# Kernel optimization log

Hardware: AMD Instinct MI355X
Metric: run time of the kernel (lower is better)

## Reference

```python
import jax, jax.numpy as jnp
import numpy as np
from jax import lax


def _quadrature_weights(bw):
    # s2cnn-style Driscoll-Healy quadrature weights over beta, length 2*bw
    j = np.arange(2 * bw)
    k = np.arange(bw)
    theta = np.pi * (2 * j + 1) / (4 * bw)
    s = (np.sin(np.outer(2 * j + 1, 2 * k + 1) * np.pi / (4 * bw)) / (2 * k + 1)).sum(-1)
    return jnp.asarray((2.0 / bw) * np.sin(theta) * s, jnp.float32)


def _conv2d(x, W, b):
    y = lax.conv_general_dilated(x, W, (1, 1), 'SAME',
                                 dimension_numbers=('NCHW', 'OIHW', 'NCHW'))
    return y + b[None, :, None, None]


def setup_inputs() -> dict:
    key = jax.random.key(0)
    ks = jax.random.split(key, 8)
    b, n = 8, 32768
    res_pt, res_r = 32, 8
    inputs = jax.random.normal(ks[0], (b, n, 3), jnp.float32)
    return {
        'inputs': inputs,
        'scale': jnp.float32(3.0),      # max radius covered by radial bins
        'sigma': jnp.float32(0.5),      # gaussian width in grid units
        'A': jnp.float32(1.0),          # splat amplitude
        'inteval_comp': jnp.float32(0.5),
        'res_pt': res_pt,
        'res_r': res_r,
        'W_s2_1': 0.08 * jax.random.normal(ks[1], (32, 8, 3, 3), jnp.float32),
        'b_s2_1': jnp.zeros((32,), jnp.float32),
        'W_s2_2': 0.05 * jax.random.normal(ks[2], (64, 32, 3, 3), jnp.float32),
        'b_s2_2': jnp.zeros((64,), jnp.float32),
        'W_gamma': 0.1 * jax.random.normal(ks[3], (64, 32), jnp.float32),
        'W_c3_1': 0.05 * jax.random.normal(ks[4], (64, 128), jnp.float32),
        'b_c3_1': jnp.zeros((64,), jnp.float32),
        'W_c3_2': 0.05 * jax.random.normal(ks[5], (32, 64), jnp.float32),
        'b_c3_2': jnp.zeros((32,), jnp.float32),
    }


def reference(inputs, scale, sigma, A, inteval_comp, res_pt, res_r,
              W_s2_1, b_s2_1, W_s2_2, b_s2_2, W_gamma,
              W_c3_1, b_c3_1, W_c3_2, b_c3_2):
    b, n, _ = inputs.shape
    # ---- remap: cartesian -> spherical with min-radius clamp (utils.remap) ----
    x, y, z = inputs[..., 0], inputs[..., 1], inputs[..., 2]
    r = jnp.maximum(jnp.sqrt(x * x + y * y + z * z), 0.1)
    theta = jnp.arccos(jnp.clip(z / r, -1.0, 1.0))            # [0, pi]
    phi = jnp.arctan2(y, x) + np.pi                            # [0, 2pi)
    # ---- s2_gridding: gaussian-weighted point -> (theta,phi,r) grid scatter ----
    ct = theta / np.pi * res_pt                                # continuous bin coords
    cp = phi / (2 * np.pi) * res_pt
    cr = r / scale * res_r
    it = jnp.clip(jnp.floor(ct).astype(jnp.int32), 0, res_pt - 1)
    ip = jnp.clip(jnp.floor(cp).astype(jnp.int32), 0, res_pt - 1)
    ir = jnp.clip(jnp.floor(cr).astype(jnp.int32), 0, res_r - 1)
    d2 = ((ct - (it + inteval_comp)) ** 2
          + (cp - (ip + inteval_comp)) ** 2
          + (cr - (ir + inteval_comp)) ** 2)
    w = A * jnp.exp(-d2 / (2.0 * sigma * sigma))               # (b, n)
    vals = jnp.stack([w, w * x, w * y, w * z], axis=-1)        # (b, n, 4)
    bidx = jnp.arange(b, dtype=jnp.int32)[:, None] * jnp.ones((1, n), jnp.int32)
    flat = ((bidx * res_pt + it) * res_pt + ip) * res_r + ir   # (b, n)
    grid = jnp.zeros((b * res_pt * res_pt * res_r, 4), jnp.float32)
    grid = grid.at[flat.reshape(-1)].add(vals.reshape(-1, 4))
    grid = grid.reshape(b, res_pt, res_pt, res_r, 4)
    ft = jnp.transpose(grid[..., 0], (0, 3, 1, 2))             # (b, res_r, res_pt, res_pt)
    # ---- encoder_l1 (s2cnn_equators): S2 convs + gamma lift to SO3 grid ----
    h = jax.nn.relu(_conv2d(ft, W_s2_1, b_s2_1))
    h = jax.nn.relu(_conv2d(h, W_s2_2, b_s2_2))                # (b, 64, res_pt, res_pt)
    ft_grid = jnp.einsum('bcxy,cg->bcxyg', h, W_gamma)         # (b, 64, rp, rp, rp)
    # ---- so3_integrate: quadrature weight over beta, sum alpha/gamma ----
    wq = _quadrature_weights(res_pt // 2)                      # (res_pt,)
    ft_max = jnp.einsum('bcxyg,y->bc', ft_grid, wq)            # (b, 64)
    # ---- broadcast global feature, concat, pointwise conv3d head ----
    ft_max_ = jnp.broadcast_to(ft_max[:, :, None, None, None],
                               (b, ft_grid.shape[1], res_pt, res_pt, res_pt))
    cat = jnp.concatenate([ft_grid, ft_max_], axis=1)          # (b, 128, rp, rp, rp)
    h3 = jax.nn.relu(jnp.einsum('bcxyg,dc->bdxyg', cat, W_c3_1)
                     + b_c3_1[None, :, None, None, None])
    out = (jnp.einsum('bdxyg,ed->bexyg', h3, W_c3_2)
           + b_c3_2[None, :, None, None, None])                # (b, 32, rp, rp, rp)
    ft_g = out.reshape(b, out.shape[1], -1).max(-1)            # (b, 32)
    return (out, ft_g)
```

## Files before the change

kernel.cpp:

```cpp
#include <hip/hip_runtime.h>
#include <math.h>

#define PI_D 3.14159265358979323846
#define PI_F 3.14159265358979323846f

typedef _Float16 half8 __attribute__((ext_vector_type(8)));
typedef _Float16 half4v __attribute__((ext_vector_type(4)));
typedef float floatx4 __attribute__((ext_vector_type(4)));
#define MFMA16(a,b,c) __builtin_amdgcn_mfma_f32_16x16x32_f16(a,b,c,0,0,0)

__global__ void k_scatter(const float* __restrict__ inp,
                          const float* __restrict__ p_scale,
                          const float* __restrict__ p_sigma,
                          const float* __restrict__ p_A,
                          const float* __restrict__ p_ic,
                          const float* __restrict__ Wg,
                          float* __restrict__ ft, float* __restrict__ wq,
                          float* __restrict__ sgs, float* __restrict__ WS) {
  int blk = blockIdx.x, t = threadIdx.x;
  if (blk == 0) {
    if (t < 32) {
      double jj = 2.0*(double)t + 1.0;
      double theta = PI_D * jj / 64.0;
      double s = 0.0;
      for (int k = 0; k < 16; ++k)
        s += sin(jj * (double)(2*k+1) * PI_D / 64.0) / (double)(2*k+1);
      wq[t] = (float)((2.0/16.0) * sin(theta) * s);
    } else if (t < 96) {
      int c = t - 32;
      float s = 0.f;
      for (int g = 0; g < 32; ++g) s += Wg[c*32 + g];
      sgs[c] = s;
    } else if (t < 224) {
      ((float4*)WS)[t - 96] = make_float4(0.f, 0.f, 0.f, 0.f);
    }
  }
  int i = blk * 256 + t;
  float scale = p_scale[0];
  float sigma = p_sigma[0];
  float A     = p_A[0];
  float icomp = p_ic[0];
  int b = i >> 15;
  float x = inp[i*3+0];
  float y = inp[i*3+1];
  float z = inp[i*3+2];
  float r = sqrtf(x*x + y*y + z*z);
  r = fmaxf(r, 0.1f);
  float ctv = fminf(fmaxf(z / r, -1.0f), 1.0f);
  float theta = acosf(ctv);
  float phi = atan2f(y, x) + PI_F;
  float ct = theta * (32.0f / PI_F);
  float cp = phi * (32.0f / (2.0f * PI_F));
  float cr = r / scale * 8.0f;
  int it = (int)floorf(ct); it = min(max(it, 0), 31);
  int ip = (int)floorf(cp); ip = min(max(ip, 0), 31);
  int ir = (int)floorf(cr); ir = min(max(ir, 0), 7);
  float dt = ct - ((float)it + icomp);
  float dp = cp - ((float)ip + icomp);
  float dr = cr - ((float)ir + icomp);
  float d2 = dt*dt + dp*dp + dr*dr;
  float w = A * expf(-d2 / (2.0f * sigma * sigma));
  atomicAdd(&ft[((b*8 + ir)*32 + it)*32 + ip], w);
}

__global__ __launch_bounds__(512) void k_conv12(
    const float* __restrict__ ft, const float* __restrict__ W1,
    const float* __restrict__ b1, const float* __restrict__ W2,
    const float* __restrict__ b2, const float* __restrict__ wq,
    const float* __restrict__ Wg, const float* __restrict__ Wc31,
    const float* __restrict__ Wc32,
    _Float16* __restrict__ VswH, _Float16* __restrict__ VswL,
    _Float16* __restrict__ W2swH, _Float16* __restrict__ W2swL,
    float* __restrict__ h2, float* __restrict__ WS) {
  __shared__ __align__(16) float ftt[8][5][32];
  __shared__ __align__(16) float h1t[32][3][32];
  __shared__ __align__(16) float W1s[72*33];
  __shared__ __align__(16) float W2s[288*65];
  int blk = blockIdx.x;
  int b = blk >> 5, xt = blk & 31;
  int t = threadIdx.x;

  {
    int flat = blk * 512 + t;
    int jj = flat & 7;
    int l  = (flat >> 3) & 63;
    int rest = flat >> 9;
    int ks = rest & 1, mt = rest >> 1;
    int c = ks*32 + (l >> 4)*8 + jj;
    int m = mt*16 + (l & 15);
    int g = m >> 6, d = m & 63;
    float val = Wg[c*32 + g] * Wc31[d*128 + c];
    _Float16 hi = (_Float16)val;
    VswH[flat] = hi;
    VswL[flat] = (_Float16)(val - (float)hi);
    if (flat < 2048) {
      int ks2 = rest & 1, mt2 = rest >> 1;
      int e = mt2*16 + (l & 15);
      int dd = ks2*32 + (l >> 4)*8 + jj;
      float v2 = Wc32[e*64 + dd];
      _Float16 h2i = (_Float16)v2;
      W2swH[flat] = h2i;
      W2swL[flat] = (_Float16)(v2 - (float)h2i);
    }
  }

  for (int idx = t; idx < 2304; idx += 512) {
    int oc2 = idx / 72, rest = idx % 72;
    W1s[rest*33 + oc2] = W1[idx];
  }
  for (int idx = t; idx < 4608; idx += 512) {
    float4 v4 = ((const float4*)W2)[idx];
    int base = idx * 4;
    int oc = base / 288, r0 = base % 288;
    W2s[(r0+0)*65 + oc] = v4.x;
    W2s[(r0+1)*65 + oc] = v4.y;
    W2s[(r0+2)*65 + oc] = v4.z;
    W2s[(r0+3)*65 + oc] = v4.w;
  }
  for (int idx = t; idx < 1280; idx += 512) {
    int y = idx & 31, xx = (idx >> 5) % 5, ic = idx / 160;
    int xg = xt + xx - 2;
    ftt[ic][xx][y] = ((unsigned)xg < 32u) ? ft[b*8192 + ic*1024 + xg*32 + y] : 0.f;
  }
  __syncthreads();

  {
    int y = t & 31, grp = t >> 5;
    float acc[2][3];
    float bb0 = b1[grp*2+0], bb1 = b1[grp*2+1];
#pragma unroll
    for (int xr = 0; xr < 3; ++xr) { acc[0][xr] = bb0; acc[1][xr] = bb1; }
    for (int ic = 0; ic < 8; ++ic) {
      float v[5][3];
#pragma unroll
      for (int dyi = 0; dyi < 3; ++dyi) {
        int yy = y + dyi - 1;
        bool ok = ((unsigned)yy < 32u);
        int yc = min(max(yy, 0), 31);
#pragma unroll
        for (int xx = 0; xx < 5; ++xx) {
          float tv = ftt[ic][xx][yc];
          v[xx][dyi] = ok ? tv : 0.f;
        }
      }
#pragma unroll
      for (int k = 0; k < 9; ++k) {
        float w0 = W1s[(ic*9 + k)*33 + grp*2];
        float w1 = W1s[(ic*9 + k)*33 + grp*2 + 1];
        int dx = k / 3, dy = k % 3;
#pragma unroll
        for (int xr = 0; xr < 3; ++xr) {
          float vv = v[xr + dx][dy];
          acc[0][xr] = fmaf(vv, w0, acc[0][xr]);
          acc[1][xr] = fmaf(vv, w1, acc[1][xr]);
        }
      }
    }
#pragma unroll
    for (int xr = 0; xr < 3; ++xr) {
      int xg = xt + xr - 1;
      bool ok = ((unsigned)xg < 32u);
      h1t[grp*2+0][xr][y] = ok ? fmaxf(acc[0][xr], 0.f) : 0.f;
      h1t[grp*2+1][xr][y] = ok ? fmaxf(acc[1][xr], 0.f) : 0.f;
    }
  }
  __syncthreads();

  {
    int y = t & 31, og = t >> 5, oc0 = og*4;
    float a0 = b2[oc0+0], a1 = b2[oc0+1], a2 = b2[oc0+2], a3 = b2[oc0+3];
    for (int ic2 = 0; ic2 < 32; ++ic2) {
      float v[3][3];
#pragma unroll
      for (int dyi = 0; dyi < 3; ++dyi) {
        int yy = y + dyi - 1;
        bool ok = ((unsigned)yy < 32u);
        int yc = min(max(yy, 0), 31);
#pragma unroll
        for (int xxi = 0; xxi < 3; ++xxi) {
          float tv = h1t[ic2][xxi][yc];
          v[xxi][dyi] = ok ? tv : 0.f;
        }
      }
#pragma unroll
      for (int k = 0; k < 9; ++k) {
        int row = (ic2*9 + k)*65 + oc0;
        float w0 = W2s[row+0], w1 = W2s[row+1], w2 = W2s[row+2], w3 = W2s[row+3];
        float vv = v[k/3][k%3];
        a0 = fmaf(vv, w0, a0);
        a1 = fmaf(vv, w1, a1);
        a2 = fmaf(vv, w2, a2);
        a3 = fmaf(vv, w3, a3);
      }
    }
    float r0 = fmaxf(a0, 0.f), r1 = fmaxf(a1, 0.f);
    float r2 = fmaxf(a2, 0.f), r3 = fmaxf(a3, 0.f);
    int pp = xt*32 + y;
    h2[(b*64 + oc0+0)*1024 + pp] = r0;
    h2[(b*64 + oc0+1)*1024 + pp] = r1;
    h2[(b*64 + oc0+2)*1024 + pp] = r2;
    h2[(b*64 + oc0+3)*1024 + pp] = r3;
    float wqv = wq[y];
    float s0 = r0*wqv, s1 = r1*wqv, s2 = r2*wqv, s3 = r3*wqv;
#pragma unroll
    for (int m = 1; m < 32; m <<= 1) {
      s0 += __shfl_xor(s0, m, 64);
      s1 += __shfl_xor(s1, m, 64);
      s2 += __shfl_xor(s2, m, 64);
      s3 += __shfl_xor(s3, m, 64);
    }
    if ((t & 31) == 0) {
      atomicAdd(&WS[b*64 + oc0+0], s0);
      atomicAdd(&WS[b*64 + oc0+1], s1);
      atomicAdd(&WS[b*64 + oc0+2], s2);
      atomicAdd(&WS[b*64 + oc0+3], s3);
    }
  }
}

__global__ __launch_bounds__(512, 4) void k_head(
    const float* __restrict__ h2, const float* __restrict__ WS,
    const float* __restrict__ sgs,
    const float* __restrict__ Wc31, const float* __restrict__ bc31,
    const float* __restrict__ bc32,
    const half8* __restrict__ VswH, const half8* __restrict__ VswL,
    const half8* __restrict__ W2swH, const half8* __restrict__ W2swL,
    float* __restrict__ out, float* __restrict__ blockmax) {
  __shared__ __align__(16) _Float16 h3H[512*72];
  __shared__ float Ks[64];
  __shared__ float vbuf2[128];
  int blk = blockIdx.x;
  int b = blk >> 6, x = (blk >> 1) & 31, h = blk & 1;
  int t = threadIdx.x;
  int lane = t & 63, w = t >> 6;
  int n16 = lane & 15, quad = lane >> 4;

  if (t < 64) {
    float acc = bc31[t];
    const float* wr = Wc31 + t*128 + 64;
    const float* wsb = WS + b*64;
    for (int c = 0; c < 64; ++c)
      acc = fmaf(wr[c], sgs[c]*wsb[c], acc);
    Ks[t] = acc;
  }

  half8 bh00, bh01, bh10, bh11, bl00, bl01, bl10, bl11;
  {
    const float* h2b = h2 + (size_t)b*64*1024 + x*32;
#pragma unroll
    for (int j = 0; j < 8; ++j) {
      int c0 = quad*8 + j;
      int c1 = 32 + c0;
      float f00 = h2b[c0*1024 + n16];
      float f01 = h2b[c1*1024 + n16];
      float f10 = h2b[c0*1024 + 16 + n16];
      float f11 = h2b[c1*1024 + 16 + n16];
      _Float16 g00 = (_Float16)f00, g01 = (_Float16)f01;
      _Float16 g10 = (_Float16)f10, g11 = (_Float16)f11;
      bh00[j] = g00;  bl00[j] = (_Float16)(f00 - (float)g00);
      bh01[j] = g01;  bl01[j] = (_Float16)(f01 - (float)g01);
      bh10[j] = g10;  bl10[j] = (_Float16)(f10 - (float)g10);
      bh11[j] = g11;  bl11[j] = (_Float16)(f11 - (float)g11);
    }
  }
  int mt2 = w & 1;
  half8 a2h0 = W2swH[(mt2*2 + 0)*64 + lane];
  half8 a2h1 = W2swH[(mt2*2 + 1)*64 + lane];
  half8 a2l0 = W2swL[(mt2*2 + 0)*64 + lane];
  half8 a2l1 = W2swL[(mt2*2 + 1)*64 + lane];
  float bias_e[4];
#pragma unroll
  for (int r = 0; r < 4; ++r) bias_e[r] = bc32[mt2*16 + quad*4 + r];
  __syncthreads();

  for (int i = 0; i < 8; ++i) {
    int mt = h*64 + w*8 + i;
    half8 ah0 = VswH[(mt*2 + 0)*64 + lane];
    half8 ah1 = VswH[(mt*2 + 1)*64 + lane];
    half8 al0 = VswL[(mt*2 + 0)*64 + lane];
    half8 al1 = VswL[(mt*2 + 1)*64 + lane];
    floatx4 acc0 = {0.f, 0.f, 0.f, 0.f};
    floatx4 acc1 = {0.f, 0.f, 0.f, 0.f};
    acc0 = MFMA16(ah0, bh00, acc0);  acc1 = MFMA16(ah0, bh10, acc1);
    acc0 = MFMA16(ah0, bl00, acc0);  acc1 = MFMA16(ah0, bl10, acc1);
    acc0 = MFMA16(al0, bh00, acc0);  acc1 = MFMA16(al0, bh10, acc1);
    acc0 = MFMA16(ah1, bh01, acc0);  acc1 = MFMA16(ah1, bh11, acc1);
    acc0 = MFMA16(ah1, bl01, acc0);  acc1 = MFMA16(ah1, bl11, acc1);
    acc0 = MFMA16(al1, bh01, acc0);  acc1 = MFMA16(al1, bh11, acc1);
    int g = mt >> 2, gl = g & 15;
    int dbase = (mt & 3)*16 + quad*4;
    float4 kv = *(const float4*)&Ks[dbase];
#pragma unroll
    for (int nt = 0; nt < 2; ++nt) {
      floatx4 a = nt ? acc1 : acc0;
      int y = nt*16 + n16;
      int rowc = y*16 + gl;
      int dsw = (dbase + y*8) & 63;
      half4v hv;
      hv[0] = (_Float16)fmaxf(a[0] + kv.x, 0.f);
      hv[1] = (_Float16)fmaxf(a[1] + kv.y, 0.f);
      hv[2] = (_Float16)fmaxf(a[2] + kv.z, 0.f);
      hv[3] = (_Float16)fmaxf(a[3] + kv.w, 0.f);
      *(half4v*)&h3H[rowc*72 + dsw] = hv;
    }
  }
  __syncthreads();
  float vmax[4] = {-3.4e38f, -3.4e38f, -3.4e38f, -3.4e38f};
  for (int i = 0; i < 8; ++i) {
    int nt2 = (w >> 1)*8 + i;
    int rowc = nt2*16 + n16;
    int dsw0 = (quad*8 + nt2*8) & 63;
    int dsw1 = (32 + quad*8 + nt2*8) & 63;
    half8 b2h0 = *(const half8*)&h3H[rowc*72 + dsw0];
    half8 b2h1 = *(const half8*)&h3H[rowc*72 + dsw1];
    floatx4 acc = {0.f, 0.f, 0.f, 0.f};
    acc = MFMA16(a2h0, b2h0, acc);
    acc = MFMA16(a2l0, b2h0, acc);
    acc = MFMA16(a2h1, b2h1, acc);
    acc = MFMA16(a2l1, b2h1, acc);
    int y = nt2, g = h*16 + n16;
    size_t base = (((size_t)(b*32 + mt2*16 + quad*4))*1024 + (size_t)(x*32 + y))*32 + g;
#pragma unroll
    for (int r = 0; r < 4; ++r) {
      float v = acc[r] + bias_e[r];
      out[base + (size_t)r*32768] = v;
      vmax[r] = fmaxf(vmax[r], v);
    }
  }
#pragma unroll
  for (int m = 1; m < 16; m <<= 1) {
#pragma unroll
    for (int r = 0; r < 4; ++r)
      vmax[r] = fmaxf(vmax[r], __shfl_xor(vmax[r], m, 64));
  }
  if (n16 == 0) {
#pragma unroll
    for (int r = 0; r < 4; ++r) vbuf2[w*16 + quad*4 + r] = vmax[r];
  }
  __syncthreads();
  if (t < 32) {
    int e = t, m2 = e >> 4, el = e & 15;
    float mm = fmaxf(fmaxf(vbuf2[(m2+0)*16 + el], vbuf2[(m2+2)*16 + el]),
                     fmaxf(vbuf2[(m2+4)*16 + el], vbuf2[(m2+6)*16 + el]));
    blockmax[blk*32 + e] = mm;
  }
}

__global__ void k_final(const float* __restrict__ blockmax, float* __restrict__ ftg) {
  int t = threadIdx.x;
  int b = t >> 5, e = t & 31;
  float m = -3.4e38f;
  for (int s = 0; s < 64; ++s) m = fmaxf(m, blockmax[(b*64 + s)*32 + e]);
  ftg[b*32 + e] = m;
}

extern "C" void kernel_launch(void* const* d_in, const int* in_sizes, int n_in,
                              void* d_out, int out_size, void* d_ws, size_t ws_size,
                              hipStream_t stream) {
  const float* inputs = (const float*)d_in[0];
  const float* scale  = (const float*)d_in[1];
  const float* sigma  = (const float*)d_in[2];
  const float* A      = (const float*)d_in[3];
  const float* icmp   = (const float*)d_in[4];
  const float* W1   = (const float*)d_in[7];
  const float* b1   = (const float*)d_in[8];
  const float* W2   = (const float*)d_in[9];
  const float* b2   = (const float*)d_in[10];
  const float* Wg   = (const float*)d_in[11];
  const float* Wc31 = (const float*)d_in[12];
  const float* bc31 = (const float*)d_in[13];
  const float* Wc32 = (const float*)d_in[14];
  const float* bc32 = (const float*)d_in[15];

  float* ws    = (float*)d_ws;
  float* ft    = ws;
  float* h2    = ws + 327680;
  float* WS    = ws + 851968;
  float* bmax  = ws + 852480;
  float* wq    = ws + 885248;
  float* sgs   = ws + 885280;
  _Float16* VswH  = (_Float16*)(ws + 885344);
  _Float16* VswL  = (_Float16*)(ws + 950880);
  _Float16* W2swH = (_Float16*)(ws + 1016416);
  _Float16* W2swL = (_Float16*)(ws + 1017440);
  float* out   = (float*)d_out;
  float* ftg   = out + 8388608;

  hipMemsetAsync(ft, 0, 65536*sizeof(float), stream);
  k_scatter<<<1024, 256, 0, stream>>>(inputs, scale, sigma, A, icmp, Wg,
                                      ft, wq, sgs, WS);
  k_conv12<<<256, 512, 0, stream>>>(ft, W1, b1, W2, b2, wq, Wg, Wc31, Wc32,
                                    VswH, VswL, W2swH, W2swL, h2, WS);
  k_head<<<512, 512, 0, stream>>>(h2, WS, sgs, Wc31, bc31, bc32,
                                  (const half8*)VswH, (const half8*)VswL,
                                  (const half8*)W2swH, (const half8*)W2swL,
                                  out, bmax);
  k_final<<<1, 256, 0, stream>>>(bmax, ftg);
}
```

Measured before the change: 167.4 us.

## Store h2 as pre-swizzled fp16 hi/lo fragments and vectorize conv weight loads

conv12 now writes its second-layer output directly as fp16 hi/lo split values, in the MFMA fragment layout that the head kernel consumes. The head can then load half8 vectors instead of doing strided fp32 gathers and converting per block. Conv weight tables in shared memory are padded to 34/68 so float2/float4 loads are possible. The quadrature-weight and Ks setup loops are also spread across more threads with shuffle reductions. The risk is bank conflicts from the new padding and extra conversion work in conv12.

```diff
diff --git a/kernel.cpp b/kernel.cpp
--- a/kernel.cpp
+++ b/kernel.cpp
@@ -19,20 +19,25 @@
                           float* __restrict__ sgs, float* __restrict__ WS) {
   int blk = blockIdx.x, t = threadIdx.x;
   if (blk == 0) {
-    if (t < 32) {
-      double jj = 2.0*(double)t + 1.0;
-      double theta = PI_D * jj / 64.0;
-      double s = 0.0;
-      for (int k = 0; k < 16; ++k)
-        s += sin(jj * (double)(2*k+1) * PI_D / 64.0) / (double)(2*k+1);
-      wq[t] = (float)((2.0/16.0) * sin(theta) * s);
-    } else if (t < 96) {
-      int c = t - 32;
+    double jj = 2.0*(double)(t >> 3) + 1.0;
+    int kk = t & 7;
+    double s = 0.0;
+#pragma unroll
+    for (int u = 0; u < 2; ++u) {
+      double k2 = (double)(2*(kk + 8*u) + 1);
+      s += sin(jj * k2 * (PI_D/64.0)) / k2;
+    }
+    s += __shfl_xor(s, 1, 64);
+    s += __shfl_xor(s, 2, 64);
+    s += __shfl_xor(s, 4, 64);
+    if (kk == 0) wq[t >> 3] = (float)((2.0/16.0) * sin(PI_D * jj / 64.0) * s);
+  } else if (blk == 1) {
+    if (t < 64) {
       float s = 0.f;
-      for (int g = 0; g < 32; ++g) s += Wg[c*32 + g];
-      sgs[c] = s;
-    } else if (t < 224) {
-      ((float4*)WS)[t - 96] = make_float4(0.f, 0.f, 0.f, 0.f);
+      for (int g = 0; g < 32; ++g) s += Wg[t*32 + g];
+      sgs[t] = s;
+    } else if (t < 192) {
+      ((float4*)WS)[t - 64] = make_float4(0.f, 0.f, 0.f, 0.f);
     }
   }
   int i = blk * 256 + t;
@@ -71,11 +76,12 @@
     const float* __restrict__ Wc32,
     _Float16* __restrict__ VswH, _Float16* __restrict__ VswL,
     _Float16* __restrict__ W2swH, _Float16* __restrict__ W2swL,
-    float* __restrict__ h2, float* __restrict__ WS) {
+    _Float16* __restrict__ h2H, _Float16* __restrict__ h2L,
+    float* __restrict__ WS) {
   __shared__ __align__(16) float ftt[8][5][32];
   __shared__ __align__(16) float h1t[32][3][32];
-  __shared__ __align__(16) float W1s[72*33];
-  __shared__ __align__(16) float W2s[288*65];
+  __shared__ __align__(16) float W1s[72*34];
+  __shared__ __align__(16) float W2s[288*68];
   int blk = blockIdx.x;
   int b = blk >> 5, xt = blk & 31;
   int t = threadIdx.x;
@@ -106,16 +112,16 @@
 
   for (int idx = t; idx < 2304; idx += 512) {
     int oc2 = idx / 72, rest = idx % 72;
-    W1s[rest*33 + oc2] = W1[idx];
+    W1s[rest*34 + oc2] = W1[idx];
   }
   for (int idx = t; idx < 4608; idx += 512) {
     float4 v4 = ((const float4*)W2)[idx];
     int base = idx * 4;
     int oc = base / 288, r0 = base % 288;
-    W2s[(r0+0)*65 + oc] = v4.x;
-    W2s[(r0+1)*65 + oc] = v4.y;
-    W2s[(r0+2)*65 + oc] = v4.z;
-    W2s[(r0+3)*65 + oc] = v4.w;
+    W2s[(r0+0)*68 + oc] = v4.x;
+    W2s[(r0+1)*68 + oc] = v4.y;
+    W2s[(r0+2)*68 + oc] = v4.z;
+    W2s[(r0+3)*68 + oc] = v4.w;
   }
   for (int idx = t; idx < 1280; idx += 512) {
     int y = idx & 31, xx = (idx >> 5) % 5, ic = idx / 160;
@@ -145,14 +151,13 @@
       }
 #pragma unroll
       for (int k = 0; k < 9; ++k) {
-        float w0 = W1s[(ic*9 + k)*33 + grp*2];
-        float w1 = W1s[(ic*9 + k)*33 + grp*2 + 1];
+        float2 w01 = *(const float2*)&W1s[(ic*9 + k)*34 + grp*2];
         int dx = k / 3, dy = k % 3;
 #pragma unroll
         for (int xr = 0; xr < 3; ++xr) {
           float vv = v[xr + dx][dy];
-          acc[0][xr] = fmaf(vv, w0, acc[0][xr]);
-          acc[1][xr] = fmaf(vv, w1, acc[1][xr]);
+          acc[0][xr] = fmaf(vv, w01.x, acc[0][xr]);
+          acc[1][xr] = fmaf(vv, w01.y, acc[1][xr]);
         }
       }
     }
@@ -184,22 +189,25 @@
       }
 #pragma unroll
       for (int k = 0; k < 9; ++k) {
-        int row = (ic2*9 + k)*65 + oc0;
-        float w0 = W2s[row+0], w1 = W2s[row+1], w2 = W2s[row+2], w3 = W2s[row+3];
+        float4 wv = *(const float4*)&W2s[(ic2*9 + k)*68 + oc0];
         float vv = v[k/3][k%3];
-        a0 = fmaf(vv, w0, a0);
-        a1 = fmaf(vv, w1, a1);
-        a2 = fmaf(vv, w2, a2);
-        a3 = fmaf(vv, w3, a3);
+        a0 = fmaf(vv, wv.x, a0);
+        a1 = fmaf(vv, wv.y, a1);
+        a2 = fmaf(vv, wv.z, a2);
+        a3 = fmaf(vv, wv.w, a3);
       }
     }
     float r0 = fmaxf(a0, 0.f), r1 = fmaxf(a1, 0.f);
     float r2 = fmaxf(a2, 0.f), r3 = fmaxf(a3, 0.f);
-    int pp = xt*32 + y;
-    h2[(b*64 + oc0+0)*1024 + pp] = r0;
-    h2[(b*64 + oc0+1)*1024 + pp] = r1;
-    h2[(b*64 + oc0+2)*1024 + pp] = r2;
-    h2[(b*64 + oc0+3)*1024 + pp] = r3;
+    int ks = og >> 3, quad = (og >> 1) & 3, jb = (og & 1) * 4;
+    int fidx = (((b*32 + xt)*2 + ks)*4 + quad)*32 + y;
+    half4v hv, lv;
+    hv[0] = (_Float16)r0; lv[0] = (_Float16)(r0 - (float)hv[0]);
+    hv[1] = (_Float16)r1; lv[1] = (_Float16)(r1 - (float)hv[1]);
+    hv[2] = (_Float16)r2; lv[2] = (_Float16)(r2 - (float)hv[2]);
+    hv[3] = (_Float16)r3; lv[3] = (_Float16)(r3 - (float)hv[3]);
+    *(half4v*)&h2H[(size_t)fidx*8 + jb] = hv;
+    *(half4v*)&h2L[(size_t)fidx*8 + jb] = lv;
     float wqv = wq[y];
     float s0 = r0*wqv, s1 = r1*wqv, s2 = r2*wqv, s3 = r3*wqv;
 #pragma unroll
@@ -219,8 +227,8 @@
 }
 
 __global__ __launch_bounds__(512, 4) void k_head(
-    const float* __restrict__ h2, const float* __restrict__ WS,
-    const float* __restrict__ sgs,
+    const _Float16* __restrict__ h2H, const _Float16* __restrict__ h2L,
+    const float* __restrict__ WS, const float* __restrict__ sgs,
     const float* __restrict__ Wc31, const float* __restrict__ bc31,
     const float* __restrict__ bc32,
     const half8* __restrict__ VswH, const half8* __restrict__ VswL,
@@ -235,33 +243,29 @@
   int lane = t & 63, w = t >> 6;
   int n16 = lane & 15, quad = lane >> 4;
 
-  if (t < 64) {
-    float acc = bc31[t];
-    const float* wr = Wc31 + t*128 + 64;
-    const float* wsb = WS + b*64;
-    for (int c = 0; c < 64; ++c)
-      acc = fmaf(wr[c], sgs[c]*wsb[c], acc);
-    Ks[t] = acc;
+  if (t < 256) {
+    int d = t >> 2, q = t & 3;
+    const float* wr  = Wc31 + d*128 + 64 + q*16;
+    const float* sg  = sgs + q*16;
+    const float* wsb = WS + b*64 + q*16;
+    float acc = 0.f;
+#pragma unroll
+    for (int c = 0; c < 16; ++c)
+      acc = fmaf(wr[c], sg[c]*wsb[c], acc);
+    acc += __shfl_xor(acc, 1, 64);
+    acc += __shfl_xor(acc, 2, 64);
+    if (q == 0) Ks[d] = acc + bc31[d];
   }
 
   half8 bh00, bh01, bh10, bh11, bl00, bl01, bl10, bl11;
   {
-    const float* h2b = h2 + (size_t)b*64*1024 + x*32;
-#pragma unroll
-    for (int j = 0; j < 8; ++j) {
-      int c0 = quad*8 + j;
-      int c1 = 32 + c0;
-      float f00 = h2b[c0*1024 + n16];
-      float f01 = h2b[c1*1024 + n16];
-      float f10 = h2b[c0*1024 + 16 + n16];
-      float f11 = h2b[c1*1024 + 16 + n16];
-      _Float16 g00 = (_Float16)f00, g01 = (_Float16)f01;
-      _Float16 g10 = (_Float16)f10, g11 = (_Float16)f11;
-      bh00[j] = g00;  bl00[j] = (_Float16)(f00 - (float)g00);
-      bh01[j] = g01;  bl01[j] = (_Float16)(f01 - (float)g01);
-      bh10[j] = g10;  bl10[j] = (_Float16)(f10 - (float)g10);
-      bh11[j] = g11;  bl11[j] = (_Float16)(f11 - (float)g11);
-    }
+    const half8* H8 = (const half8*)h2H;
+    const half8* L8 = (const half8*)h2L;
+    int fo = ((b*32 + x)*8 + quad)*32;
+    bh00 = H8[fo + n16];        bh10 = H8[fo + 16 + n16];
+    bl00 = L8[fo + n16];        bl10 = L8[fo + 16 + n16];
+    bh01 = H8[fo + 128 + n16];  bh11 = H8[fo + 128 + 16 + n16];
+    bl01 = L8[fo + 128 + n16];  bl11 = L8[fo + 128 + 16 + n16];
   }
   int mt2 = w & 1;
   half8 a2h0 = W2swH[(mt2*2 + 0)*64 + lane];
@@ -374,15 +378,16 @@
 
   float* ws    = (float*)d_ws;
   float* ft    = ws;
-  float* h2    = ws + 327680;
-  float* WS    = ws + 851968;
-  float* bmax  = ws + 852480;
-  float* wq    = ws + 885248;
-  float* sgs   = ws + 885280;
-  _Float16* VswH  = (_Float16*)(ws + 885344);
-  _Float16* VswL  = (_Float16*)(ws + 950880);
-  _Float16* W2swH = (_Float16*)(ws + 1016416);
-  _Float16* W2swL = (_Float16*)(ws + 1017440);
+  _Float16* h2H = (_Float16*)(ws + 65536);
+  _Float16* h2L = (_Float16*)(ws + 327680);
+  float* WS    = ws + 589824;
+  float* bmax  = ws + 590336;
+  float* wq    = ws + 606720;
+  float* sgs   = ws + 606752;
+  _Float16* VswH  = (_Float16*)(ws + 606816);
+  _Float16* VswL  = (_Float16*)(ws + 672352);
+  _Float16* W2swH = (_Float16*)(ws + 737888);
+  _Float16* W2swL = (_Float16*)(ws + 738912);
   float* out   = (float*)d_out;
   float* ftg   = out + 8388608;
 
@@ -390,8 +395,8 @@
   k_scatter<<<1024, 256, 0, stream>>>(inputs, scale, sigma, A, icmp, Wg,
                                       ft, wq, sgs, WS);
   k_conv12<<<256, 512, 0, stream>>>(ft, W1, b1, W2, b2, wq, Wg, Wc31, Wc32,
-                                    VswH, VswL, W2swH, W2swL, h2, WS);
-  k_head<<<512, 512, 0, stream>>>(h2, WS, sgs, Wc31, bc31, bc32,
+                                    VswH, VswL, W2swH, W2swL, h2H, h2L, WS);
+  k_head<<<512, 512, 0, stream>>>(h2H, h2L, WS, sgs, Wc31, bc31, bc32,
                                   (const half8*)VswH, (const half8*)VswL,
                                   (const half8*)W2swH, (const half8*)W2swL,
                                   out, bmax);
```

Result: faster. 163.5 us (-2.3%).
